# Kernel optimization log

Hardware: AMD Instinct MI355X
Metric: run time of the kernel (lower is better)

The kernel has to match this reference:

```python
import jax, jax.numpy as jnp
import numpy as np

ALPHA = 0.2  # leaky relu slope
NEG_INF = -1.0e12


def _gat(x, adj, W, a):
    # x: [N, Fin], W: [Fin, Fout], a: [2*Fout, 1]
    h = x @ W                                  # [N, Fout]
    Fout = W.shape[1]
    # additive attention: e_ij = leakyrelu(h_i . a[:Fout] + h_j . a[Fout:])
    f1 = h @ a[:Fout, 0]                       # [N]
    f2 = h @ a[Fout:, 0]                       # [N]
    e = jax.nn.leaky_relu(f1[:, None] + f2[None, :], ALPHA)  # [N, N]
    att = jnp.where(adj > 0, e, NEG_INF)
    att = jax.nn.softmax(att, axis=1)          # dropout=0 -> identity
    return jax.nn.elu(att @ h + h)             # [N, Fout]


def setup_inputs() -> dict:
    key = jax.random.key(0)
    k = jax.random.split(key, 6)
    N, NFEAT, NHID, NNEXT = 8192, 256, 128, 1024
    x = jax.random.normal(k[0], (N, NFEAT), dtype=jnp.float32)
    adj = (jax.random.uniform(k[1], (N, N)) > 0.9).astype(jnp.float32)
    # xavier-uniform-ish init
    def xav(kk, shape):
        lim = np.sqrt(6.0 / (shape[0] + shape[1])) * 1.414
        return jax.random.uniform(kk, shape, minval=-lim, maxval=lim, dtype=jnp.float32)
    W_embed = xav(k[2], (NFEAT, NHID))
    a_embed = xav(k[3], (2 * NHID, 1))
    W_assign = xav(k[4], (NFEAT, NNEXT))
    a_assign = xav(k[5], (2 * NNEXT, 1))
    return {"x": x, "adj": adj, "W_embed": W_embed, "a_embed": a_embed,
            "W_assign": W_assign, "a_assign": a_assign}


def reference(x, adj, W_embed, a_embed, W_assign, a_assign):
    z_l = _gat(x, adj, W_embed, a_embed)          # [N, nhid]
    assign = _gat(x, adj, W_assign, a_assign)     # [N, nnext]
    s_l = jax.nn.softmax(assign, axis=-1)         # [N, nnext]
    xnext = s_l.T @ z_l                            # [nnext, nhid]
    anext = s_l.T @ adj @ s_l                      # [nnext, nnext]
    return xnext, anext, s_l
```

## Files before the change

### kernel.cpp

```cpp
#include <hip/hip_runtime.h>
#include <hip/hip_bf16.h>


#define DI __device__ __forceinline__

typedef __attribute__((ext_vector_type(8))) short short8;
typedef __attribute__((ext_vector_type(4))) float f32x4;

static DI float bf2f(short s) {
    union { unsigned u; float f; } c;
    c.u = ((unsigned)(unsigned short)s) << 16;
    return c.f;
}
static DI short f2bf(float f) {
    union { float f; unsigned u; } c; c.f = f;
    unsigned r = (c.u + 0x7FFFu + ((c.u >> 16) & 1u)) >> 16;
    return (short)(unsigned short)r;
}
static DI short f2bf_tr(float f) {
    union { float f; unsigned u; } c; c.f = f;
    return (short)(unsigned short)(c.u >> 16);
}
template <int F32>
static DI short8 ld8(const void* base, size_t off) {
    if (F32 == 0) return *(const short8*)((const short*)base + off);
    const float* p = (const float*)base + off;
    f32x4 a = *(const f32x4*)p;
    f32x4 b = *(const f32x4*)(p + 4);
    short8 v;
    #pragma unroll
    for (int e = 0; e < 4; e++) { v[e] = f2bf(a[e]); v[4 + e] = f2bf(b[e]); }
    return v;
}
static DI float wred_sum(float v) {
    #pragma unroll
    for (int o = 32; o > 0; o >>= 1) v += __shfl_down(v, o, 64);
    return v;
}
static DI float wred_max(float v) {
    #pragma unroll
    for (int o = 32; o > 0; o >>= 1) v = fmaxf(v, __shfl_down(v, o, 64));
    return v;
}
static DI int sfun(int r) { return (r ^ (r >> 3)) & 7; }
static DI int swzk(int k, int r) {
    return (k & ~63) | ((((k >> 3) & 7) ^ sfun(r)) << 3) | (k & 7);
}
static DI unsigned pack2(short lo, short hi) {
    return ((unsigned)(unsigned short)lo) | (((unsigned)(unsigned short)hi) << 16);
}
static DI void gload16(const void* g, void* l) {
    __builtin_amdgcn_global_load_lds(
        (const __attribute__((address_space(1))) unsigned int*)g,
        (__attribute__((address_space(3))) unsigned int*)l, 16, 0, 0);
}

template <int EPI, int SWZX>
__launch_bounds__(256)
__global__ void gemm_lds(const short* __restrict__ A, const short* __restrict__ Bt,
                         void* __restrict__ C, int ldc, int kcount) {
    __shared__ short As0[128][64], Bs0[128][64];
    __shared__ short As1[128][64], Bs1[128][64];
    int bx = blockIdx.x, by = blockIdx.y;
    if (SWZX) {
        int lid = blockIdx.x + blockIdx.y * 8;
        int c = lid & 7, s = lid >> 3;
        by = c * 8 + (s >> 3);
        bx = s & 7;
    }
    const int tid  = threadIdx.x;
    const int lane = tid & 63;
    const int w    = tid >> 6;
    const int wr   = w >> 1, wc = w & 1;
    const int i0   = by * 128;
    const int n0   = bx * 128;
    const int k0   = blockIdx.z * kcount;

    const int srow = w * 32 + (lane >> 3);
    const short* gA = A  + (size_t)(i0 + srow) * 8192 + k0 + (lane & 7) * 8;
    const short* gB = Bt + (size_t)(n0 + srow) * 8192 + k0 + (lane & 7) * 8;

    f32x4 acc[4][4];
    #pragma unroll
    for (int m = 0; m < 4; m++)
        #pragma unroll
        for (int n = 0; n < 4; n++) acc[m][n] = (f32x4){0.f, 0.f, 0.f, 0.f};

#define STAGE_TILE(ts, Ab, Bb)                                                  \
    do {                                                                        \
        _Pragma("unroll")                                                       \
        for (int j = 0; j < 4; j++) {                                           \
            gload16(gA + (size_t)(ts) * 64 + (size_t)j * 8 * 8192,              \
                    &Ab[w * 32 + j * 8][0]);                                    \
            gload16(gB + (size_t)(ts) * 64 + (size_t)j * 8 * 8192,              \
                    &Bb[w * 32 + j * 8][0]);                                    \
        }                                                                       \
    } while (0)

#define COMPUTE_TILE(Ab, Bb)                                                    \
    do {                                                                        \
        _Pragma("unroll")                                                       \
        for (int kk = 0; kk < 2; kk++) {                                        \
            short8 af[4], bq[4];                                                \
            _Pragma("unroll")                                                   \
            for (int m = 0; m < 4; m++) {                                       \
                int ar = wr * 64 + m * 16 + (lane & 15);                        \
                af[m] = *(const short8*)&Ab[ar]                                 \
                            [swzk(kk * 32 + (lane >> 4) * 8, ar)];              \
            }                                                                   \
            _Pragma("unroll")                                                   \
            for (int n = 0; n < 4; n++) {                                       \
                int br = wc * 64 + n * 16 + (lane & 15);                        \
                bq[n] = *(const short8*)&Bb[br]                                 \
                            [swzk(kk * 32 + (lane >> 4) * 8, br)];              \
            }                                                                   \
            _Pragma("unroll")                                                   \
            for (int m = 0; m < 4; m++)                                         \
                _Pragma("unroll")                                               \
                for (int n = 0; n < 4; n++)                                     \
                    acc[m][n] = __builtin_amdgcn_mfma_f32_16x16x32_bf16(        \
                        af[m], bq[n], acc[m][n], 0, 0, 0);                      \
        }                                                                       \
    } while (0)

    const int nt = kcount >> 6;
    STAGE_TILE(0, As0, Bs0);
    for (int t = 0; t < nt; t += 2) {
        __syncthreads();
        STAGE_TILE(t + 1, As1, Bs1);
        COMPUTE_TILE(As0, Bs0);
        __syncthreads();
        if (t + 2 < nt) STAGE_TILE(t + 2, As0, Bs0);
        COMPUTE_TILE(As1, Bs1);
    }
#undef STAGE_TILE
#undef COMPUTE_TILE

    #pragma unroll
    for (int m = 0; m < 4; m++) {
        #pragma unroll
        for (int n = 0; n < 4; n++) {
            int row0 = i0 + wr * 64 + m * 16 + ((lane >> 4) << 2);
            int col  = n0 + wc * 64 + n * 16 + (lane & 15);
            if (EPI == 1) {
                unsigned long long pk = 0;
                #pragma unroll
                for (int r = 0; r < 4; r++)
                    pk |= (unsigned long long)(unsigned short)f2bf(acc[m][n][r])
                          << (16 * r);
                *(unsigned long long*)((short*)C + (size_t)col * 8192 +
                                       swzk(row0, col)) = pk;
            } else {
                #pragma unroll
                for (int r = 0; r < 4; r++) {
                    float v = acc[m][n][r];
                    if (EPI == 0) ((float*)C)[(size_t)(row0 + r) * ldc + col] = v;
                    else atomicAdd(&((float*)C)[(size_t)(row0 + r) * ldc + col], v);
                }
            }
        }
    }
}

template <int SWZX>
__launch_bounds__(256)
__global__ void gemm_xw_k(const float* __restrict__ A, const float* __restrict__ B,
                          short* __restrict__ C, short* __restrict__ Ct, int ldn) {
    __shared__ short As[128][64];
    __shared__ short Bs[128][64];
    int bx = blockIdx.x, by = blockIdx.y;
    if (SWZX) {
        int lid = blockIdx.x + blockIdx.y * 8;
        int c = lid & 7, s = lid >> 3;
        by = c * 8 + (s >> 3);
        bx = s & 7;
    }
    const int tid  = threadIdx.x;
    const int lane = tid & 63;
    const int w    = tid >> 6;
    const int wr   = w >> 1, wc = w & 1;
    const int i0   = by * 128;
    const int n0   = bx * 128;

    f32x4 acc[4][4];
    #pragma unroll
    for (int m = 0; m < 4; m++)
        #pragma unroll
        for (int n = 0; n < 4; n++) acc[m][n] = (f32x4){0.f, 0.f, 0.f, 0.f};

    for (int ks = 0; ks < 256; ks += 64) {
        __syncthreads();
        #pragma unroll
        for (int it = 0; it < 4; it++) {
            int idx = it * 256 + tid;
            int cg = idx & 7, r = idx >> 3;
            *(short8*)&As[r][swzk(cg * 8, r)] =
                ld8<1>(A, (size_t)(i0 + r) * 256 + ks + cg * 8);
        }
        #pragma unroll
        for (int it = 0; it < 2; it++) {
            int idx = it * 256 + tid;
            int ng = idx & 15, kp = idx >> 4;
            int k = 2 * kp;
            short8 r0 = ld8<1>(B, (size_t)(ks + k) * ldn + n0 + ng * 8);
            short8 r1 = ld8<1>(B, (size_t)(ks + k + 1) * ldn + n0 + ng * 8);
            #pragma unroll
            for (int j = 0; j < 8; j++) {
                int row = ng * 8 + j;
                *(unsigned*)&Bs[row][swzk(k, row)] = pack2(r0[j], r1[j]);
            }
        }
        __syncthreads();
        #pragma unroll
        for (int kk = 0; kk < 2; kk++) {
            short8 af[4], bq[4];
            #pragma unroll
            for (int m = 0; m < 4; m++) {
                int ar = wr * 64 + m * 16 + (lane & 15);
                af[m] = *(const short8*)&As[ar][swzk(kk * 32 + (lane >> 4) * 8, ar)];
            }
            #pragma unroll
            for (int n = 0; n < 4; n++) {
                int br = wc * 64 + n * 16 + (lane & 15);
                bq[n] = *(const short8*)&Bs[br][swzk(kk * 32 + (lane >> 4) * 8, br)];
            }
            #pragma unroll
            for (int m = 0; m < 4; m++)
                #pragma unroll
                for (int n = 0; n < 4; n++)
                    acc[m][n] = __builtin_amdgcn_mfma_f32_16x16x32_bf16(
                        af[m], bq[n], acc[m][n], 0, 0, 0);
        }
    }
    #pragma unroll
    for (int m = 0; m < 4; m++) {
        #pragma unroll
        for (int n = 0; n < 4; n++) {
            int row0 = i0 + wr * 64 + m * 16 + ((lane >> 4) << 2);
            int col  = n0 + wc * 64 + n * 16 + (lane & 15);
            unsigned long long pk = 0;
            #pragma unroll
            for (int r = 0; r < 4; r++) {
                short b = f2bf(acc[m][n][r]);
                C[(size_t)(row0 + r) * ldn + col] = b;
                pk |= (unsigned long long)(unsigned short)b << (16 * r);
            }
            *(unsigned long long*)(Ct + (size_t)col * 8192 + swzk(row0, col)) = pk;
        }
    }
}

__launch_bounds__(256)
__global__ void compute_f_k(const short* __restrict__ h1, const short* __restrict__ h2,
                            const float* __restrict__ ae, const float* __restrict__ aa,
                            float* __restrict__ f11, float* __restrict__ f21,
                            float* __restrict__ f12, float* __restrict__ f22) {
    int row = blockIdx.x, t = threadIdx.x;
    float s11 = 0.f, s21 = 0.f, s12 = 0.f, s22 = 0.f;
    if (t < 128) {
        float hv = bf2f(h1[(size_t)row * 128 + t]);
        s11 = hv * ae[t];
        s21 = hv * ae[128 + t];
    }
    #pragma unroll
    for (int q = 0; q < 4; q++) {
        int f = t + q * 256;
        float hv = bf2f(h2[(size_t)row * 1024 + f]);
        s12 += hv * aa[f];
        s22 += hv * aa[1024 + f];
    }
    __shared__ float red[4][4];
    s11 = wred_sum(s11); s21 = wred_sum(s21);
    s12 = wred_sum(s12); s22 = wred_sum(s22);
    int w = t >> 6;
    if ((t & 63) == 0) { red[0][w] = s11; red[1][w] = s21; red[2][w] = s12; red[3][w] = s22; }
    __syncthreads();
    if (t == 0) {
        f11[row] = red[0][0] + red[0][1] + red[0][2] + red[0][3];
        f21[row] = red[1][0] + red[1][1] + red[1][2] + red[1][3];
        f12[row] = red[2][0] + red[2][1] + red[2][2] + red[2][3];
        f22[row] = red[3][0] + red[3][1] + red[3][2] + red[3][3];
    }
}

__launch_bounds__(256)
__global__ void evec_k(const float* __restrict__ f11, const float* __restrict__ f21,
                       const float* __restrict__ f12, const float* __restrict__ f22,
                       float* __restrict__ E11, float* __restrict__ F11,
                       float* __restrict__ E21, float* __restrict__ F21,
                       float* __restrict__ E12, float* __restrict__ F12,
                       float* __restrict__ E22, float* __restrict__ F22) {
    int i = blockIdx.x * 256 + threadIdx.x;
    if (i >= 8192) return;
    float a = f11[i], b = f21[i], c = f12[i], d = f22[i];
    E11[i] = __expf(a); F11[i] = __expf(0.2f * a);
    E21[i] = __expf(b); F21[i] = __expf(0.2f * b);
    E12[i] = __expf(c); F12[i] = __expf(0.2f * c);
    E22[i] = __expf(d); F22[i] = __expf(0.2f * d);
}

__launch_bounds__(256)
__global__ void prepass_k(const float* __restrict__ adj,
                          const float* __restrict__ E11, const float* __restrict__ F11,
                          const float* __restrict__ E21, const float* __restrict__ F21,
                          const float* __restrict__ E12, const float* __restrict__ F12,
                          const float* __restrict__ E22, const float* __restrict__ F22,
                          float* __restrict__ den1, float* __restrict__ den2,
                          short* __restrict__ adjb, short* __restrict__ P1b,
                          short* __restrict__ P2b) {
    int row = blockIdx.x, t = threadIdx.x;
    float e1r = E11[row], f1r = F11[row];
    float e2r = E12[row], f2r = F12[row];
    float d1 = 0.f, d2 = 0.f;
    const float* arow = adj + (size_t)row * 8192;
    #pragma unroll
    for (int it = 0; it < 4; it++) {
        int jb = (it * 256 + t) * 8;
        size_t wo = (size_t)row * 8192 + swzk(jb, row);
        f32x4 a0 = *(const f32x4*)(arow + jb), a1 = *(const f32x4*)(arow + jb + 4);
        f32x4 eA0 = *(const f32x4*)(E21 + jb), eA1 = *(const f32x4*)(E21 + jb + 4);
        f32x4 fA0 = *(const f32x4*)(F21 + jb), fA1 = *(const f32x4*)(F21 + jb + 4);
        f32x4 eB0 = *(const f32x4*)(E22 + jb), eB1 = *(const f32x4*)(E22 + jb + 4);
        f32x4 fB0 = *(const f32x4*)(F22 + jb), fB1 = *(const f32x4*)(F22 + jb + 4);
        short8 ab, p1v, p2v;
        #pragma unroll
        for (int e = 0; e < 8; e++) {
            float av = e < 4 ? a0[e] : a1[e - 4];
            float eA = e < 4 ? eA0[e] : eA1[e - 4];
            float fA = e < 4 ? fA0[e] : fA1[e - 4];
            float eB = e < 4 ? eB0[e] : eB1[e - 4];
            float fB = e < 4 ? fB0[e] : fB1[e - 4];
            float aa = e1r * eA, bb = f1r * fA;
            float x1 = aa > 1.f ? aa : bb;
            float cc = e2r * eB, dd = f2r * fB;
            float x2 = cc > 1.f ? cc : dd;
            float p1 = av > 0.f ? x1 : 0.f;
            float p2 = av > 0.f ? x2 : 0.f;
            d1 += p1; d2 += p2;
            ab[e] = f2bf_tr(av); p1v[e] = f2bf(p1); p2v[e] = f2bf(p2);
        }
        *(short8*)(adjb + wo) = ab;
        *(short8*)(P1b  + wo) = p1v;
        *(short8*)(P2b  + wo) = p2v;
    }
    __shared__ float r1[4], r2[4];
    d1 = wred_sum(d1); d2 = wred_sum(d2);
    if ((t & 63) == 0) { r1[t >> 6] = d1; r2[t >> 6] = d2; }
    __syncthreads();
    if (t == 0) {
        den1[row] = r1[0] + r1[1] + r1[2] + r1[3];
        den2[row] = r2[0] + r2[1] + r2[2] + r2[3];
    }
}

__launch_bounds__(256)
__global__ void epi_gat1_k(const float* __restrict__ Y1, const float* __restrict__ den1,
                           const short* __restrict__ h1, short* __restrict__ zl) {
    int idx = blockIdx.x * 256 + threadIdx.x;
    int base = idx * 8;
    int row = base >> 7;
    float d = den1[row]; d = d > 0.f ? d : 1.f;
    f32x4 y0 = *(const f32x4*)(Y1 + base), y1 = *(const f32x4*)(Y1 + base + 4);
    short8 hv = *(const short8*)(h1 + base);
    short8 o;
    #pragma unroll
    for (int e = 0; e < 8; e++) {
        float z = (e < 4 ? y0[e] : y1[e - 4]) / d + bf2f(hv[e]);
        z = z > 0.f ? z : (__expf(z) - 1.f);
        o[e] = f2bf(z);
    }
    *(short8*)(zl + base) = o;
}

__launch_bounds__(256)
__global__ void episoft_k(const float* __restrict__ Y2, const float* __restrict__ den2,
                          const short* __restrict__ h2, float* __restrict__ slo,
                          short* __restrict__ slb) {
    int row = blockIdx.x, t = threadIdx.x;
    float d = den2[row];
    d = d > 0.f ? d : 1.f;
    float v[4], mx = -1e30f;
    #pragma unroll
    for (int q = 0; q < 4; q++) {
        int j = t + q * 256;
        float a = Y2[(size_t)row * 1024 + j] / d + bf2f(h2[(size_t)row * 1024 + j]);
        a = a > 0.f ? a : (__expf(a) - 1.f);
        v[q] = a;
        mx = fmaxf(mx, a);
    }
    __shared__ float sred[4];
    __shared__ float sbc;
    mx = wred_max(mx);
    if ((t & 63) == 0) sred[t >> 6] = mx;
    __syncthreads();
    if (t == 0) sbc = fmaxf(fmaxf(sred[0], sred[1]), fmaxf(sred[2], sred[3]));
    __syncthreads();
    mx = sbc;
    float s = 0.f;
    #pragma unroll
    for (int q = 0; q < 4; q++) { v[q] = __expf(v[q] - mx); s += v[q]; }
    s = wred_sum(s);
    if ((t & 63) == 0) sred[t >> 6] = s;
    __syncthreads();
    if (t == 0) sbc = sred[0] + sred[1] + sred[2] + sred[3];
    __syncthreads();
    float inv = 1.f / sbc;
    #pragma unroll
    for (int q = 0; q < 4; q++) {
        float sv = v[q] * inv;
        slo[(size_t)row * 1024 + t + q * 256] = sv;
        slb[(size_t)row * 1024 + t + q * 256] = f2bf(sv);
    }
}

template <int F32IN>
__launch_bounds__(256)
__global__ void transpose_swz_k(const void* __restrict__ in, short* __restrict__ out,
                                int R, int C) {
    __shared__ short ts[64][72];
    int tc = blockIdx.x * 64;
    int tr = blockIdx.y * 64;
    int t = threadIdx.x;
    #pragma unroll
    for (int h = 0; h < 2; h++) {
        int r = (t >> 3) + h * 32, c = (t & 7) * 8;
        *(short8*)&ts[r][c] = ld8<F32IN>(in, (size_t)(tr + r) * C + tc + c);
    }
    __syncthreads();
    #pragma unroll
    for (int h = 0; h < 2; h++) {
        int n = t >> 2, blk = (t & 3) + h * 4;
        short8 v;
        #pragma unroll
        for (int e = 0; e < 8; e++) v[e] = ts[blk * 8 + e][n];
        *(short8*)(out + (size_t)(tc + n) * R + tr + ((blk ^ sfun(tc + n)) << 3)) = v;
    }
}

extern "C" void kernel_launch(void* const* d_in, const int* in_sizes, int n_in,
                              void* d_out, int out_size, void* d_ws, size_t ws_size,
                              hipStream_t stream) {
    const float* x   = (const float*)d_in[0];
    const float* adj = (const float*)d_in[1];
    const float* We  = (const float*)d_in[2];
    const float* ae  = (const float*)d_in[3];
    const float* Wa  = (const float*)d_in[4];
    const float* aa  = (const float*)d_in[5];
    float* out = (float*)d_out;

    char* w = (char*)d_ws;
    short* h1b = (short*)(w);
    short* h2b = (short*)(w + (2u   << 20));
    float* f11 = (float*)(w + (18u  << 20));
    float* f21 = f11 + 8192;  float* f12 = f21 + 8192; float* f22 = f12 + 8192;
    float* den1 = f22 + 8192; float* den2 = den1 + 8192;
    float* E11 = den2 + 8192; float* F11 = E11 + 8192;
    float* E21 = F11 + 8192;  float* F21 = E21 + 8192;
    float* E12 = F21 + 8192;  float* F12 = E12 + 8192;
    float* E22 = F12 + 8192;  float* F22 = E22 + 8192;
    short* zl  = (short*)(w + (19u << 20));
    float* Y1f = (float*)(w + (21u << 20));
    float* Y2f = (float*)(w + (25u << 20));
    short* slb = (short*)(w + (57u << 20));
    short* h1t = (short*)(w + (73u << 20));
    short* h2t = (short*)(w + (75u << 20));
    short* slt = (short*)(w + (91u << 20));
    short* zlt = (short*)(w + (107u << 20));
    short* tT  = (short*)(w + (109u << 20));
    short* adjb = (short*)(w + (128u << 20));
    short* P1b  = (short*)(w + (256u << 20));
    short* P2b  = (short*)(w + (384u << 20));

    float* xo  = out;
    float* ao  = out + 131072;
    float* slo = out + 131072 + 1048576;

    hipMemsetAsync(out, 0, (size_t)(131072 + 1048576) * 4, stream);
    hipMemsetAsync(Y1f, 0, (size_t)8192 * 128 * 4, stream);

    gemm_xw_k<0><<<dim3(1, 64), 256, 0, stream>>>(x, We, h1b, h1t, 128);
    gemm_xw_k<1><<<dim3(8, 64), 256, 0, stream>>>(x, Wa, h2b, h2t, 1024);
    compute_f_k<<<dim3(8192), 256, 0, stream>>>(h1b, h2b, ae, aa, f11, f21, f12, f22);
    evec_k<<<dim3(32), 256, 0, stream>>>(f11, f21, f12, f22,
        E11, F11, E21, F21, E12, F12, E22, F22);
    prepass_k<<<dim3(8192), 256, 0, stream>>>(adj,
        E11, F11, E21, F21, E12, F12, E22, F22, den1, den2, adjb, P1b, P2b);

    gemm_lds<3, 0><<<dim3(1, 64, 8), 256, 0, stream>>>(P1b, h1t, Y1f, 128, 1024);
    epi_gat1_k<<<dim3(512), 256, 0, stream>>>(Y1f, den1, h1b, zl);
    transpose_swz_k<0><<<dim3(2, 128), 256, 0, stream>>>(zl, zlt, 8192, 128);

    gemm_lds<0, 1><<<dim3(8, 64, 1), 256, 0, stream>>>(P2b, h2t, Y2f, 1024, 8192);
    episoft_k<<<dim3(8192), 256, 0, stream>>>(Y2f, den2, h2b, slo, slb);
    transpose_swz_k<0><<<dim3(16, 128), 256, 0, stream>>>(slb, slt, 8192, 1024);

    gemm_lds<1, 1><<<dim3(8, 64, 1), 256, 0, stream>>>(adjb, slt, tT, 0, 8192);

    gemm_lds<3, 0><<<dim3(8, 8, 8), 256, 0, stream>>>(slt, tT, ao, 1024, 1024);
    gemm_lds<3, 0><<<dim3(1, 8, 32), 256, 0, stream>>>(slt, zlt, xo, 128, 256);
}
```

Baseline: 748.0 us.

## Deepen GEMM LDS pipeline to four buffers with partial vmcnt waits

Replaces the double-buffered LDS pipeline in the bf16 MFMA GEMM with a 4-stage ring buffer that keeps three tiles of global-to-LDS loads in flight. Each iteration waits on a partial vmcnt count plus a raw barrier instead of a full __syncthreads, so memory latency can overlap more compute. LDS use doubles to 128KB per block, which may lower occupancy. The raw waits also depend on the exact number of outstanding loads per stage.

```diff
diff --git a/kernel.cpp b/kernel.cpp
--- a/kernel.cpp
+++ b/kernel.cpp
@@ -54,13 +54,20 @@
         (const __attribute__((address_space(1))) unsigned int*)g,
         (__attribute__((address_space(3))) unsigned int*)l, 16, 0, 0);
 }
+static DI void pb_wait(int cnt) {
+    if (cnt == 16)     asm volatile("s_waitcnt vmcnt(16)" ::: "memory");
+    else if (cnt == 8) asm volatile("s_waitcnt vmcnt(8)"  ::: "memory");
+    else               asm volatile("s_waitcnt vmcnt(0)"  ::: "memory");
+    __builtin_amdgcn_s_barrier();
+    __builtin_amdgcn_sched_barrier(0);
+}
 
 template <int EPI, int SWZX>
 __launch_bounds__(256)
 __global__ void gemm_lds(const short* __restrict__ A, const short* __restrict__ Bt,
                          void* __restrict__ C, int ldc, int kcount) {
-    __shared__ short As0[128][64], Bs0[128][64];
-    __shared__ short As1[128][64], Bs1[128][64];
+    __shared__ short As[4][128][64];
+    __shared__ short Bs[4][128][64];
     int bx = blockIdx.x, by = blockIdx.y;
     if (SWZX) {
         int lid = blockIdx.x + blockIdx.y * 8;
@@ -86,18 +93,18 @@
         #pragma unroll
         for (int n = 0; n < 4; n++) acc[m][n] = (f32x4){0.f, 0.f, 0.f, 0.f};
 
-#define STAGE_TILE(ts, Ab, Bb)                                                  \
+#define STAGE_TILE(ts, buf)                                                     \
     do {                                                                        \
         _Pragma("unroll")                                                       \
         for (int j = 0; j < 4; j++) {                                           \
             gload16(gA + (size_t)(ts) * 64 + (size_t)j * 8 * 8192,              \
-                    &Ab[w * 32 + j * 8][0]);                                    \
+                    &As[buf][w * 32 + j * 8][0]);                               \
             gload16(gB + (size_t)(ts) * 64 + (size_t)j * 8 * 8192,              \
-                    &Bb[w * 32 + j * 8][0]);                                    \
+                    &Bs[buf][w * 32 + j * 8][0]);                               \
         }                                                                       \
     } while (0)
 
-#define COMPUTE_TILE(Ab, Bb)                                                    \
+#define COMPUTE_TILE(buf)                                                       \
     do {                                                                        \
         _Pragma("unroll")                                                       \
         for (int kk = 0; kk < 2; kk++) {                                        \
@@ -105,13 +112,13 @@
             _Pragma("unroll")                                                   \
             for (int m = 0; m < 4; m++) {                                       \
                 int ar = wr * 64 + m * 16 + (lane & 15);                        \
-                af[m] = *(const short8*)&Ab[ar]                                 \
+                af[m] = *(const short8*)&As[buf][ar]                            \
                             [swzk(kk * 32 + (lane >> 4) * 8, ar)];              \
             }                                                                   \
             _Pragma("unroll")                                                   \
             for (int n = 0; n < 4; n++) {                                       \
                 int br = wc * 64 + n * 16 + (lane & 15);                        \
-                bq[n] = *(const short8*)&Bb[br]                                 \
+                bq[n] = *(const short8*)&Bs[buf][br]                            \
                             [swzk(kk * 32 + (lane >> 4) * 8, br)];              \
             }                                                                   \
             _Pragma("unroll")                                                   \
@@ -124,14 +131,13 @@
     } while (0)
 
     const int nt = kcount >> 6;
-    STAGE_TILE(0, As0, Bs0);
-    for (int t = 0; t < nt; t += 2) {
-        __syncthreads();
-        STAGE_TILE(t + 1, As1, Bs1);
-        COMPUTE_TILE(As0, Bs0);
-        __syncthreads();
-        if (t + 2 < nt) STAGE_TILE(t + 2, As0, Bs0);
-        COMPUTE_TILE(As1, Bs1);
+    STAGE_TILE(0, 0);
+    STAGE_TILE(1, 1);
+    STAGE_TILE(2, 2);
+    for (int t = 0; t < nt; t++) {
+        pb_wait(t + 2 < nt ? 16 : (t + 1 < nt ? 8 : 0));
+        if (t + 3 < nt) STAGE_TILE(t + 3, (t + 3) & 3);
+        COMPUTE_TILE(t & 3);
     }
 #undef STAGE_TILE
 #undef COMPUTE_TILE
```

After: 1.130 ms. +51.1%, slower.

## Generate GAT1 attention weights inside GEMM and fuse epilogue with transpose

Applied to the files above, without the earlier changes.

The prepass no longer writes the 128MB bf16 P1 matrix. The first GAT aggregation GEMM now builds its attention weights on the fly from the bf16 adjacency and the E/F vectors while staging A tiles into LDS. The ELU epilogue for z_l is also fused with the swizzled transpose, so the separate transpose kernel and the zl buffer go away. This cuts a large HBM write and read, but adds ALU work and register-staged A loads inside the GEMM loop, which may weaken its pipelining.

```diff
diff --git a/kernel.cpp b/kernel.cpp
--- a/kernel.cpp
+++ b/kernel.cpp
@@ -134,7 +134,6 @@
         COMPUTE_TILE(As1, Bs1);
     }
 #undef STAGE_TILE
-#undef COMPUTE_TILE
 
     #pragma unroll
     for (int m = 0; m < 4; m++) {
@@ -160,6 +159,135 @@
             }
         }
     }
+#undef COMPUTE_TILE
+}
+
+template <int EPI>
+__launch_bounds__(256)
+__global__ void gemm_gen(const short* __restrict__ Ab, const short* __restrict__ Bt,
+                         float* __restrict__ C, int ldc, int kcount,
+                         const float* __restrict__ E1, const float* __restrict__ F1,
+                         const float* __restrict__ E2, const float* __restrict__ F2) {
+    __shared__ short As0[128][64], Bs0[128][64];
+    __shared__ short As1[128][64], Bs1[128][64];
+    const int tid  = threadIdx.x;
+    const int lane = tid & 63;
+    const int w    = tid >> 6;
+    const int wr   = w >> 1, wc = w & 1;
+    const int i0   = blockIdx.y * 128;
+    const int n0   = blockIdx.x * 128;
+    const int k0   = blockIdx.z * kcount;
+
+    const int srow = w * 32 + (lane >> 3);
+    const short* gB = Bt + (size_t)(n0 + srow) * 8192 + k0 + (lane & 7) * 8;
+
+    f32x4 acc[4][4];
+    #pragma unroll
+    for (int m = 0; m < 4; m++)
+        #pragma unroll
+        for (int n = 0; n < 4; n++) acc[m][n] = (f32x4){0.f, 0.f, 0.f, 0.f};
+
+    short8 avr[4];
+
+#define G_ALOAD(ts)                                                             \
+    do {                                                                        \
+        _Pragma("unroll")                                                       \
+        for (int it = 0; it < 4; it++) {                                        \
+            int idx = it * 256 + tid;                                           \
+            int r = idx >> 3, kb = idx & 7;                                     \
+            avr[it] = *(const short8*)(Ab + (size_t)(i0 + r) * 8192 + k0 +      \
+                                       (size_t)(ts) * 64 + kb * 8);             \
+        }                                                                       \
+    } while (0)
+
+#define G_BLOAD(ts, Bb)                                                         \
+    do {                                                                        \
+        _Pragma("unroll")                                                       \
+        for (int j = 0; j < 4; j++)                                             \
+            gload16(gB + (size_t)(ts) * 64 + (size_t)j * 8 * 8192,              \
+                    &Bb[w * 32 + j * 8][0]);                                    \
+    } while (0)
+
+#define G_WSTAGE(ts, As_)                                                       \
+    do {                                                                        \
+        _Pragma("unroll")                                                       \
+        for (int it = 0; it < 4; it++) {                                        \
+            int idx = it * 256 + tid;                                           \
+            int r = idx >> 3, kb = idx & 7;                                     \
+            int kl = k0 + (ts) * 64 + ((kb ^ sfun(r)) << 3);                    \
+            float e1r = E1[i0 + r], f1r = F1[i0 + r];                           \
+            f32x4 e2a = *(const f32x4*)(E2 + kl);                               \
+            f32x4 e2b = *(const f32x4*)(E2 + kl + 4);                           \
+            f32x4 f2a = *(const f32x4*)(F2 + kl);                               \
+            f32x4 f2b = *(const f32x4*)(F2 + kl + 4);                           \
+            short8 av = avr[it], p;                                             \
+            _Pragma("unroll")                                                   \
+            for (int e = 0; e < 8; e++) {                                       \
+                float ev = e < 4 ? e2a[e] : e2b[e - 4];                         \
+                float fv = e < 4 ? f2a[e] : f2b[e - 4];                         \
+                float wg = fmaxf(e1r * ev, f1r * fv);                           \
+                p[e] = ((unsigned short)av[e]) ? f2bf(wg) : (short)0;           \
+            }                                                                   \
+            *(short8*)&As_[r][kb * 8] = p;                                      \
+        }                                                                       \
+    } while (0)
+
+#define G_COMPUTE(Ab_, Bb_)                                                     \
+    do {                                                                        \
+        _Pragma("unroll")                                                       \
+        for (int kk = 0; kk < 2; kk++) {                                        \
+            short8 af[4], bq[4];                                                \
+            _Pragma("unroll")                                                   \
+            for (int m = 0; m < 4; m++) {                                       \
+                int ar = wr * 64 + m * 16 + (lane & 15);                        \
+                af[m] = *(const short8*)&Ab_[ar]                                \
+                            [swzk(kk * 32 + (lane >> 4) * 8, ar)];              \
+            }                                                                   \
+            _Pragma("unroll")                                                   \
+            for (int n = 0; n < 4; n++) {                                       \
+                int br = wc * 64 + n * 16 + (lane & 15);                        \
+                bq[n] = *(const short8*)&Bb_[br]                                \
+                            [swzk(kk * 32 + (lane >> 4) * 8, br)];              \
+            }                                                                   \
+            _Pragma("unroll")                                                   \
+            for (int m = 0; m < 4; m++)                                         \
+                _Pragma("unroll")                                               \
+                for (int n = 0; n < 4; n++)                                     \
+                    acc[m][n] = __builtin_amdgcn_mfma_f32_16x16x32_bf16(        \
+                        af[m], bq[n], acc[m][n], 0, 0, 0);                      \
+        }                                                                       \
+    } while (0)
+
+    const int nt = kcount >> 6;
+    G_ALOAD(0);
+    G_BLOAD(0, Bs0);
+    for (int t = 0; t < nt; t += 2) {
+        G_WSTAGE(t, As0);
+        __syncthreads();
+        G_ALOAD(t + 1);
+        G_BLOAD(t + 1, Bs1);
+        G_COMPUTE(As0, Bs0);
+        G_WSTAGE(t + 1, As1);
+        __syncthreads();
+        if (t + 2 < nt) { G_ALOAD(t + 2); G_BLOAD(t + 2, Bs0); }
+        G_COMPUTE(As1, Bs1);
+    }
+#undef G_ALOAD
+#undef G_BLOAD
+#undef G_WSTAGE
+#undef G_COMPUTE
+
+    #pragma unroll
+    for (int m = 0; m < 4; m++) {
+        #pragma unroll
+        for (int n = 0; n < 4; n++) {
+            int row0 = i0 + wr * 64 + m * 16 + ((lane >> 4) << 2);
+            int col  = n0 + wc * 64 + n * 16 + (lane & 15);
+            #pragma unroll
+            for (int r = 0; r < 4; r++)
+                atomicAdd(&C[(size_t)(row0 + r) * ldc + col], acc[m][n][r]);
+        }
+    }
 }
 
 template <int SWZX>
@@ -306,8 +434,7 @@
                           const float* __restrict__ E12, const float* __restrict__ F12,
                           const float* __restrict__ E22, const float* __restrict__ F22,
                           float* __restrict__ den1, float* __restrict__ den2,
-                          short* __restrict__ adjb, short* __restrict__ P1b,
-                          short* __restrict__ P2b) {
+                          short* __restrict__ adjb, short* __restrict__ P2b) {
     int row = blockIdx.x, t = threadIdx.x;
     float e1r = E11[row], f1r = F11[row];
     float e2r = E12[row], f2r = F12[row];
@@ -322,7 +449,7 @@
         f32x4 fA0 = *(const f32x4*)(F21 + jb), fA1 = *(const f32x4*)(F21 + jb + 4);
         f32x4 eB0 = *(const f32x4*)(E22 + jb), eB1 = *(const f32x4*)(E22 + jb + 4);
         f32x4 fB0 = *(const f32x4*)(F22 + jb), fB1 = *(const f32x4*)(F22 + jb + 4);
-        short8 ab, p1v, p2v;
+        short8 ab, p2v;
         #pragma unroll
         for (int e = 0; e < 8; e++) {
             float av = e < 4 ? a0[e] : a1[e - 4];
@@ -330,17 +457,14 @@
             float fA = e < 4 ? fA0[e] : fA1[e - 4];
             float eB = e < 4 ? eB0[e] : eB1[e - 4];
             float fB = e < 4 ? fB0[e] : fB1[e - 4];
-            float aa = e1r * eA, bb = f1r * fA;
-            float x1 = aa > 1.f ? aa : bb;
-            float cc = e2r * eB, dd = f2r * fB;
-            float x2 = cc > 1.f ? cc : dd;
+            float x1 = fmaxf(e1r * eA, f1r * fA);
+            float x2 = fmaxf(e2r * eB, f2r * fB);
             float p1 = av > 0.f ? x1 : 0.f;
             float p2 = av > 0.f ? x2 : 0.f;
             d1 += p1; d2 += p2;
-            ab[e] = f2bf_tr(av); p1v[e] = f2bf(p1); p2v[e] = f2bf(p2);
+            ab[e] = f2bf_tr(av); p2v[e] = f2bf(p2);
         }
         *(short8*)(adjb + wo) = ab;
-        *(short8*)(P1b  + wo) = p1v;
         *(short8*)(P2b  + wo) = p2v;
     }
     __shared__ float r1[4], r2[4];
@@ -354,22 +478,35 @@
 }
 
 __launch_bounds__(256)
-__global__ void epi_gat1_k(const float* __restrict__ Y1, const float* __restrict__ den1,
-                           const short* __restrict__ h1, short* __restrict__ zl) {
-    int idx = blockIdx.x * 256 + threadIdx.x;
-    int base = idx * 8;
-    int row = base >> 7;
-    float d = den1[row]; d = d > 0.f ? d : 1.f;
-    f32x4 y0 = *(const f32x4*)(Y1 + base), y1 = *(const f32x4*)(Y1 + base + 4);
-    short8 hv = *(const short8*)(h1 + base);
-    short8 o;
-    #pragma unroll
-    for (int e = 0; e < 8; e++) {
-        float z = (e < 4 ? y0[e] : y1[e - 4]) / d + bf2f(hv[e]);
-        z = z > 0.f ? z : (__expf(z) - 1.f);
-        o[e] = f2bf(z);
-    }
-    *(short8*)(zl + base) = o;
+__global__ void epi_gat1t_k(const float* __restrict__ Y1, const float* __restrict__ den1,
+                            const short* __restrict__ h1, short* __restrict__ zlt) {
+    __shared__ short ts[128][65];
+    int tr = blockIdx.x * 64;
+    int t = threadIdx.x;
+    #pragma unroll
+    for (int it = 0; it < 4; it++) {
+        int idx = it * 256 + t;
+        int r = idx >> 4, cb = idx & 15;
+        int row = tr + r;
+        float d = den1[row]; d = d > 0.f ? d : 1.f;
+        const float* yp = Y1 + (size_t)row * 128 + cb * 8;
+        f32x4 y0 = *(const f32x4*)yp, y1 = *(const f32x4*)(yp + 4);
+        short8 hv = *(const short8*)(h1 + (size_t)row * 128 + cb * 8);
+        #pragma unroll
+        for (int e = 0; e < 8; e++) {
+            float z = (e < 4 ? y0[e] : y1[e - 4]) / d + bf2f(hv[e]);
+            z = z > 0.f ? z : (__expf(z) - 1.f);
+            ts[cb * 8 + e][r] = f2bf(z);
+        }
+    }
+    __syncthreads();
+    #pragma unroll
+    for (int it = 0; it < 4; it++) {
+        int idx = it * 256 + t;
+        int c = idx >> 3, rb = idx & 7;
+        short8 v = *(const short8*)&ts[c][rb * 8];
+        *(short8*)(zlt + (size_t)c * 8192 + tr + ((rb ^ sfun(c)) << 3)) = v;
+    }
 }
 
 __launch_bounds__(256)
@@ -458,7 +595,6 @@
     float* E21 = F11 + 8192;  float* F21 = E21 + 8192;
     float* E12 = F21 + 8192;  float* F12 = E12 + 8192;
     float* E22 = F12 + 8192;  float* F22 = E22 + 8192;
-    short* zl  = (short*)(w + (19u << 20));
     float* Y1f = (float*)(w + (21u << 20));
     float* Y2f = (float*)(w + (25u << 20));
     short* slb = (short*)(w + (57u << 20));
@@ -468,8 +604,7 @@
     short* zlt = (short*)(w + (107u << 20));
     short* tT  = (short*)(w + (109u << 20));
     short* adjb = (short*)(w + (128u << 20));
-    short* P1b  = (short*)(w + (256u << 20));
-    short* P2b  = (short*)(w + (384u << 20));
+    short* P2b  = (short*)(w + (256u << 20));
 
     float* xo  = out;
     float* ao  = out + 131072;
@@ -484,11 +619,11 @@
     evec_k<<<dim3(32), 256, 0, stream>>>(f11, f21, f12, f22,
         E11, F11, E21, F21, E12, F12, E22, F22);
     prepass_k<<<dim3(8192), 256, 0, stream>>>(adj,
-        E11, F11, E21, F21, E12, F12, E22, F22, den1, den2, adjb, P1b, P2b);
-
-    gemm_lds<3, 0><<<dim3(1, 64, 8), 256, 0, stream>>>(P1b, h1t, Y1f, 128, 1024);
-    epi_gat1_k<<<dim3(512), 256, 0, stream>>>(Y1f, den1, h1b, zl);
-    transpose_swz_k<0><<<dim3(2, 128), 256, 0, stream>>>(zl, zlt, 8192, 128);
+        E11, F11, E21, F21, E12, F12, E22, F22, den1, den2, adjb, P2b);
+
+    gemm_gen<3><<<dim3(1, 64, 8), 256, 0, stream>>>(
+        adjb, h1t, Y1f, 128, 1024, E11, F11, E21, F21);
+    epi_gat1t_k<<<dim3(128), 256, 0, stream>>>(Y1f, den1, h1b, zlt);
 
     gemm_lds<0, 1><<<dim3(8, 64, 1), 256, 0, stream>>>(P2b, h2t, Y2f, 1024, 8192);
     episoft_k<<<dim3(8192), 256, 0, stream>>>(Y2f, den2, h2b, slo, slb);
```

Measured after the change: 723.4 us. 3.3% less time.
